# Kernel tuning notes

Measured on AMD Instinct MI355X. Metric: run time of the kernel, lower is better.

## Reference

```python
import jax, jax.numpy as jnp
import numpy as np

FEAT_STRIDE = 16
SCALES = np.array([8.0, 16.0, 32.0])
RATIOS = np.array([0.5, 1.0, 2.0])
PRE_NMS_TOP_N = 6000
POST_NMS_TOP_N = 300
NMS_THRESH = 0.7


def _whctrs(anchor):
    w = anchor[2] - anchor[0] + 1.0
    h = anchor[3] - anchor[1] + 1.0
    cx = anchor[0] + 0.5 * (w - 1.0)
    cy = anchor[1] + 0.5 * (h - 1.0)
    return w, h, cx, cy


def _mkanchors(ws, hs, cx, cy):
    return np.stack([cx - 0.5 * (ws - 1.0), cy - 0.5 * (hs - 1.0),
                     cx + 0.5 * (ws - 1.0), cy + 0.5 * (hs - 1.0)], axis=1)


def generate_anchors(base_size=16, ratios=RATIOS, scales=SCALES):
    base = np.array([0.0, 0.0, base_size - 1.0, base_size - 1.0])
    w, h, cx, cy = _whctrs(base)
    size = w * h
    ws = np.round(np.sqrt(size / ratios))
    hs = np.round(ws * ratios)
    ratio_anchors = _mkanchors(ws, hs, cx, cy)
    out = []
    for a in ratio_anchors:
        w, h, cx, cy = _whctrs(a)
        out.append(_mkanchors(w * scales, h * scales, cx, cy))
    return np.vstack(out)  # (A=9, 4)


def setup_inputs():
    key = jax.random.key(0)
    k1, k2 = jax.random.split(key)
    B, A, H, W = 8, 9, 152, 152
    scores_in = jax.random.normal(k1, (B, 2 * A, H, W), jnp.float32)
    bbox_deltas = 0.5 * jax.random.normal(k2, (B, 4 * A, H, W), jnp.float32)
    im_info = jnp.tile(jnp.array([[H * FEAT_STRIDE, W * FEAT_STRIDE, 1.0]], jnp.float32), (B, 1))
    anchors = jnp.asarray(generate_anchors(), jnp.float32)
    return {"scores_in": scores_in, "bbox_deltas": bbox_deltas, "im_info": im_info, "anchors": anchors}


def bbox_transform_inv(boxes, deltas):
    w = boxes[..., 2] - boxes[..., 0] + 1.0
    h = boxes[..., 3] - boxes[..., 1] + 1.0
    cx = boxes[..., 0] + 0.5 * w
    cy = boxes[..., 1] + 0.5 * h
    dx, dy, dw, dh = deltas[..., 0], deltas[..., 1], deltas[..., 2], deltas[..., 3]
    pcx = dx * w + cx
    pcy = dy * h + cy
    pw = jnp.exp(dw) * w
    ph = jnp.exp(dh) * h
    return jnp.stack([pcx - 0.5 * pw, pcy - 0.5 * ph, pcx + 0.5 * pw, pcy + 0.5 * ph], axis=-1)


def clip_boxes(boxes, im_info):
    wmax = im_info[:, None, 1] - 1.0  # x bound, per image
    hmax = im_info[:, None, 0] - 1.0  # y bound
    x1 = jnp.minimum(jnp.maximum(boxes[..., 0], 0.0), wmax)
    y1 = jnp.minimum(jnp.maximum(boxes[..., 1], 0.0), hmax)
    x2 = jnp.minimum(jnp.maximum(boxes[..., 2], 0.0), wmax)
    y2 = jnp.minimum(jnp.maximum(boxes[..., 3], 0.0), hmax)
    return jnp.stack([x1, y1, x2, y2], axis=-1)


def nms_indices(boxes, thresh, max_out):
    # boxes: (N, 4), sorted by score descending. Greedy NMS -> up to max_out indices, -1 padded.
    x1, y1, x2, y2 = boxes[:, 0], boxes[:, 1], boxes[:, 2], boxes[:, 3]
    areas = (x2 - x1 + 1.0) * (y2 - y1 + 1.0)
    N = boxes.shape[0]

    def body(i, carry):
        suppressed, keep = carry
        idx = jnp.argmax(~suppressed)  # first surviving box = highest remaining score
        valid = ~suppressed[idx]
        keep = keep.at[i].set(jnp.where(valid, idx.astype(jnp.int32), -1))
        xx1 = jnp.maximum(x1[idx], x1)
        yy1 = jnp.maximum(y1[idx], y1)
        xx2 = jnp.minimum(x2[idx], x2)
        yy2 = jnp.minimum(y2[idx], y2)
        inter = jnp.maximum(xx2 - xx1 + 1.0, 0.0) * jnp.maximum(yy2 - yy1 + 1.0, 0.0)
        iou = inter / (areas[idx] + areas - inter)
        suppressed = jnp.where(valid, suppressed | (iou > thresh), suppressed)
        return suppressed, keep

    _, keep = jax.lax.fori_loop(0, max_out, body,
                                (jnp.zeros(N, bool), jnp.full(max_out, -1, jnp.int32)))
    return keep


def _forward(scores_in, bbox_deltas, im_info, anchors):
    B, _, H, W = scores_in.shape
    A = anchors.shape[0]
    # fg objectness scores: channels [A:2A] -> (B, K*A) in (row, col, anchor) order
    scores = scores_in[:, A:].transpose(0, 2, 3, 1).reshape(B, -1)
    deltas = bbox_deltas.transpose(0, 2, 3, 1).reshape(B, -1, 4)
    sx = (jnp.arange(W) * FEAT_STRIDE).astype(jnp.float32)
    sy = (jnp.arange(H) * FEAT_STRIDE).astype(jnp.float32)
    gx, gy = jnp.meshgrid(sx, sy)  # (H, W)
    shifts = jnp.stack([gx.ravel(), gy.ravel(), gx.ravel(), gy.ravel()], axis=1)  # (K, 4)
    all_anchors = (anchors[None, :, :] + shifts[:, None, :]).reshape(-1, 4)  # (K*A, 4)
    proposals = bbox_transform_inv(all_anchors[None], deltas)  # (B, K*A, 4)
    proposals = clip_boxes(proposals, im_info)
    _, order = jax.lax.top_k(scores, PRE_NMS_TOP_N)  # descending, == sorted order truncated
    props_top = jnp.take_along_axis(proposals, order[..., None], axis=1)  # (B, PRE, 4)
    keep = jax.vmap(lambda b: nms_indices(b, NMS_THRESH, POST_NMS_TOP_N))(props_top)  # (B, POST)
    valid = keep >= 0
    sel = jnp.take_along_axis(props_top, jnp.maximum(keep, 0)[..., None], axis=1)
    sel = jnp.where(valid[..., None], sel, 0.0)
    batch_col = jnp.broadcast_to(jnp.arange(B, dtype=jnp.float32)[:, None, None],
                                 (B, POST_NMS_TOP_N, 1))
    return jnp.concatenate([batch_col, sel], axis=2)  # (B, POST, 5)


def reference(scores_in, bbox_deltas, im_info, anchors):
    return _forward(scores_in, bbox_deltas, im_info, anchors)
```

## Files before the change

kernel.cpp:

```cpp
#include <hip/hip_runtime.h>
#include <stdint.h>

#define H_ 152
#define W_ 152
#define A_ 9
#define HW_ (H_ * W_)
#define N_ (HW_ * A_)
#define B_ 8
#define PRE_TOP 6000
#define POST_TOP 300
#define NBUCK 4096
#define NFINE 32768
#define CAND_CAP 8192
#define NMS_TH 0.7f
#define CNT_STRIDE 32
#define RTILE 512
#define DEC_PIXBLK 91
#define DEC_BLKS (72 * DEC_PIXBLK)
#define ZERO_BLKS 128

#define OFF_HIST    0
#define OFF_SSUF    131072
#define OFF_CNT     262144
#define OFF_CAND    263168
#define OFF_GROUP   787456
#define OFF_BOXES   1311744
#define OFF_BALL    2079744
#define WS_NEED     (2079744ull + 26615808ull)


__device__ __forceinline__ unsigned fkey(float f) {
    unsigned u = __float_as_uint(f);
    return (u & 0x80000000u) ? ~u : (u | 0x80000000u);
}

__device__ __forceinline__ bool sup_test(float ax1, float ay1, float ax2, float ay2, float aar,
                                         float bx1, float by1, float bx2, float by2, float bar) {
    float xx1 = fmaxf(ax1, bx1);
    float yy1 = fmaxf(ay1, by1);
    float xx2 = fminf(ax2, bx2);
    float yy2 = fminf(ay2, by2);
    float iw = fmaxf(xx2 - xx1 + 1.0f, 0.0f);
    float ih = fmaxf(yy2 - yy1 + 1.0f, 0.0f);
    float inter = __fmul_rn(iw, ih);
    float iou = inter / (aar + bar - inter);
    return iou > NMS_TH;
}

__device__ __forceinline__ float4 decode_box(float an0, float an1, float an2, float an3,
                                             float sx, float sy,
                                             float dx, float dy, float dw, float dh,
                                             float wmax, float hmax) {
    float ax1 = an0 + sx;
    float ay1 = an1 + sy;
    float ax2 = an2 + sx;
    float ay2 = an3 + sy;
    float ww = ax2 - ax1 + 1.0f;
    float hh = ay2 - ay1 + 1.0f;
    float ctx = ax1 + 0.5f * ww;
    float cty = ay1 + 0.5f * hh;
    float pcx = __fadd_rn(__fmul_rn(dx, ww), ctx);
    float pcy = __fadd_rn(__fmul_rn(dy, hh), cty);
    float pw = __fmul_rn(expf(dw), ww);
    float ph = __fmul_rn(expf(dh), hh);
    float x1 = pcx - 0.5f * pw;
    float y1 = pcy - 0.5f * ph;
    float x2 = pcx + 0.5f * pw;
    float y2 = pcy + 0.5f * ph;
    x1 = fminf(fmaxf(x1, 0.0f), wmax);
    y1 = fminf(fmaxf(y1, 0.0f), hmax);
    x2 = fminf(fmaxf(x2, 0.0f), wmax);
    y2 = fminf(fmaxf(y2, 0.0f), hmax);
    return make_float4(x1, y1, x2, y2);
}


__global__ void init_k(const float* __restrict__ deltas,
                       const float* __restrict__ anchors,
                       const float* __restrict__ im_info,
                       float4* __restrict__ ball,
                       unsigned* __restrict__ zbase, unsigned* __restrict__ zboxes,
                       int nDecBlks) {
    int bid = blockIdx.x;
    if (bid < nDecBlks) {
        int ba = bid / DEC_PIXBLK;
        int b = ba / A_, a = ba - (ba / A_) * A_;
        int pix = (bid % DEC_PIXBLK) * 256 + threadIdx.x;
        if (pix >= HW_) return;
        const float* db = deltas + ((size_t)b * 36 + 4 * a) * HW_;
        float dx = db[pix];
        float dy = db[pix + HW_];
        float dw = db[pix + 2 * HW_];
        float dh = db[pix + 3 * HW_];
        float an0 = anchors[a * 4 + 0];
        float an1 = anchors[a * 4 + 1];
        float an2 = anchors[a * 4 + 2];
        float an3 = anchors[a * 4 + 3];
        float hmax = im_info[b * 3 + 0] - 1.0f;
        float wmax = im_info[b * 3 + 1] - 1.0f;
        int w = pix % W_, h = pix / W_;
        float sx = (float)(w * 16), sy = (float)(h * 16);
        ball[(size_t)b * N_ + a * HW_ + pix] =
            decode_box(an0, an1, an2, an3, sx, sy, dx, dy, dw, dh, wmax, hmax);
    } else {
        const int n1 = 263168 / 4;
        const int n2 = 768000 / 4;
        int i = (bid - nDecBlks) * 256 + (int)threadIdx.x;
        int st = ZERO_BLKS * 256;
        for (int k = i; k < n1 + n2; k += st) {
            if (k < n1) zbase[k] = 0u;
            else zboxes[k - n1] = 0u;
        }
    }
}

__global__ void hist_k(const float* __restrict__ scores, unsigned* __restrict__ hist) {
    __shared__ unsigned lh[NBUCK];
    int b = blockIdx.y;
    for (int i = threadIdx.x; i < NBUCK; i += blockDim.x) lh[i] = 0;
    __syncthreads();
    const float4* sb = (const float4*)(scores + ((size_t)b * 18 + A_) * HW_);
    const int N4 = N_ / 4;
    int stride = gridDim.x * blockDim.x;
    for (int e = blockIdx.x * blockDim.x + threadIdx.x; e < N4; e += stride) {
        float4 v = sb[e];
        atomicAdd(&lh[fkey(v.x) >> 20], 1u);
        atomicAdd(&lh[fkey(v.y) >> 20], 1u);
        atomicAdd(&lh[fkey(v.z) >> 20], 1u);
        atomicAdd(&lh[fkey(v.w) >> 20], 1u);
    }
    __syncthreads();
    for (int i = threadIdx.x; i < NBUCK; i += blockDim.x) {
        unsigned v = lh[i];
        if (v) atomicAdd(&hist[b * NBUCK + i], v);
    }
}

__global__ void scan_k(const unsigned* __restrict__ hist, unsigned* __restrict__ bucketT) {
    __shared__ unsigned ps[1024];
    int b = blockIdx.x, t = threadIdx.x;
    const unsigned* hb = hist + b * NBUCK;
    unsigned c0 = hb[4095 - (4 * t + 0)];
    unsigned c1 = hb[4095 - (4 * t + 1)];
    unsigned c2 = hb[4095 - (4 * t + 2)];
    unsigned c3 = hb[4095 - (4 * t + 3)];
    unsigned local = c0 + c1 + c2 + c3;
    ps[t] = local;
    __syncthreads();
    for (int off = 1; off < 1024; off <<= 1) {
        unsigned v = (t >= off) ? ps[t - off] : 0u;
        __syncthreads();
        ps[t] += v;
        __syncthreads();
    }
    unsigned incl = ps[t], excl = incl - local;
    if (excl < PRE_TOP && incl >= PRE_TOP) {
        unsigned cum = excl;
        unsigned cc[4] = {c0, c1, c2, c3};
#pragma unroll
        for (int k = 0; k < 4; ++k) {
            cum += cc[k];
            if (cum >= PRE_TOP) { bucketT[b] = (unsigned)(4095 - (4 * t + k)); break; }
        }
    }
    if (t == 1023 && ps[1023] < PRE_TOP) bucketT[b] = 0;
}

__global__ void compact_k(const float* __restrict__ scores, const unsigned* __restrict__ bucketT,
                          unsigned* __restrict__ cnt, uint2* __restrict__ cand) {
    __shared__ unsigned wtot[4], wbase[4];
    __shared__ unsigned blkbase;
    int b = blockIdx.y;
    const float4* sb = (const float4*)(scores + ((size_t)b * 18 + A_) * HW_);
    unsigned T = bucketT[b];
    int lane = threadIdx.x & 63;
    int wid = threadIdx.x >> 6;
    const int N4 = N_ / 4;
    int stride = gridDim.x * blockDim.x;
    int niters = (N4 + stride - 1) / stride;
    unsigned long long lower = (lane == 63) ? 0x7fffffffffffffffull
                                            : ((1ull << lane) - 1ull);
    for (int it = 0; it < niters; ++it) {
        int e = it * stride + blockIdx.x * (int)blockDim.x + (int)threadIdx.x;
        bool p0 = false, p1 = false, p2 = false, p3 = false;
        unsigned k0 = 0, k1 = 0, k2 = 0, k3 = 0;
        if (e < N4) {
            float4 v = sb[e];
            k0 = fkey(v.x); k1 = fkey(v.y); k2 = fkey(v.z); k3 = fkey(v.w);
            p0 = (k0 >> 20) >= T; p1 = (k1 >> 20) >= T;
            p2 = (k2 >> 20) >= T; p3 = (k3 >> 20) >= T;
        }
        unsigned long long m0 = __ballot(p0), m1 = __ballot(p1);
        unsigned long long m2 = __ballot(p2), m3 = __ballot(p3);
        unsigned t0 = (unsigned)__popcll(m0), t1 = (unsigned)__popcll(m1);
        unsigned t2 = (unsigned)__popcll(m2), t3 = (unsigned)__popcll(m3);
        unsigned wtotal = t0 + t1 + t2 + t3;
        if (lane == 0) wtot[wid] = wtotal;
        __syncthreads();
        if (threadIdx.x == 0) {
            unsigned s0 = wtot[0], s1 = wtot[1], s2 = wtot[2], s3 = wtot[3];
            unsigned tot = s0 + s1 + s2 + s3;
            blkbase = tot ? atomicAdd(&cnt[b * CNT_STRIDE], tot) : 0u;
            wbase[0] = 0; wbase[1] = s0; wbase[2] = s0 + s1; wbase[3] = s0 + s1 + s2;
        }
        __syncthreads();
        if (wtotal) {
            unsigned base = blkbase + wbase[wid];
            unsigned o0 = base + (unsigned)__popcll(m0 & lower);
            unsigned o1 = base + t0 + (unsigned)__popcll(m1 & lower);
            unsigned o2 = base + t0 + t1 + (unsigned)__popcll(m2 & lower);
            unsigned o3 = base + t0 + t1 + t2 + (unsigned)__popcll(m3 & lower);
            uint2* cb = cand + (size_t)b * CAND_CAP;
            int e4 = e * 4;
            if (p0 && o0 < CAND_CAP) {
                int a = (e4 + 0) / HW_, pix = (e4 + 0) - a * HW_;
                cb[o0] = make_uint2(k0, (unsigned)(pix * A_ + a));
            }
            if (p1 && o1 < CAND_CAP) {
                int a = (e4 + 1) / HW_, pix = (e4 + 1) - a * HW_;
                cb[o1] = make_uint2(k1, (unsigned)(pix * A_ + a));
            }
            if (p2 && o2 < CAND_CAP) {
                int a = (e4 + 2) / HW_, pix = (e4 + 2) - a * HW_;
                cb[o2] = make_uint2(k2, (unsigned)(pix * A_ + a));
            }
            if (p3 && o3 < CAND_CAP) {
                int a = (e4 + 3) / HW_, pix = (e4 + 3) - a * HW_;
                cb[o3] = make_uint2(k3, (unsigned)(pix * A_ + a));
            }
        }
    }
}

__global__ void __launch_bounds__(1024) finesort_k(const unsigned* __restrict__ cnt,
                                                   uint2* __restrict__ cand,
                                                   unsigned long long* __restrict__ grouped) {
    __shared__ unsigned lh[NFINE];
    __shared__ unsigned ps[1024];
    int b = blockIdx.x, t = threadIdx.x;
    int M = min((int)cnt[b * CNT_STRIDE], CAND_CAP);
    uint2* cb = cand + (size_t)b * CAND_CAP;
    unsigned long long* g = grouped + (size_t)b * CAND_CAP;
    for (int i = t; i < NFINE; i += 1024) lh[i] = 0u;
    __syncthreads();
    for (int i = t; i < M; i += 1024) {
        unsigned key16 = cb[i].x >> 16;
        unsigned f = (key16 >= 32768u) ? (key16 - 32768u) : 0u;
        atomicAdd(&lh[f], 1u);
    }
    __syncthreads();
    unsigned c[32];
    unsigned local = 0;
#pragma unroll
    for (int k = 0; k < 32; ++k) { c[k] = lh[32767 - (32 * t + k)]; local += c[k]; }
    ps[t] = local;
    __syncthreads();
    for (int off = 1; off < 1024; off <<= 1) {
        unsigned v = (t >= off) ? ps[t - off] : 0u;
        __syncthreads();
        ps[t] += v;
        __syncthreads();
    }
    unsigned run = ps[t] - local;
    __syncthreads();
#pragma unroll
    for (int k = 0; k < 32; ++k) {
        lh[32767 - (32 * t + k)] = run;
        run += c[k];
    }
    __syncthreads();
    for (int i = t; i < M; i += 1024) {
        uint2 cd = cb[i];
        unsigned key16 = cd.x >> 16;
        unsigned f = (key16 >= 32768u) ? (key16 - 32768u) : 0u;
        unsigned pos = atomicAdd(&lh[f], 1u);
        if (pos < CAND_CAP)
            g[pos] = ((unsigned long long)cd.x << 32) | (unsigned)(~cd.y);
    }
    __syncthreads();
    ushort* S16 = (ushort*)cb;
    for (int i = t; i < NFINE; i += 1024)
        S16[i] = (ushort)min(lh[i], 65535u);
}

__global__ void __launch_bounds__(256) rank_k(const unsigned* __restrict__ cnt,
                                              const unsigned long long* __restrict__ grouped,
                                              const ushort* __restrict__ S16all,
                                              const float4* __restrict__ ball,
                                              float4* __restrict__ boxes) {
    __shared__ unsigned long long tile[RTILE];
    __shared__ int s_rs, s_re;
    int b = blockIdx.y, t = threadIdx.x;
    int M = min((int)cnt[b * CNT_STRIDE], CAND_CAP);
    int c0 = blockIdx.x * 256;
    if (c0 >= M) return;
    const unsigned long long* g = grouped + (size_t)b * CAND_CAP;
    const ushort* S16 = S16all + (size_t)b * NFINE;
    int i = c0 + t;
    bool valid = i < M;
    unsigned long long comp = valid ? g[i] : 0ull;

    unsigned n = valid ? ~(unsigned)comp : 0u;
    int a = (int)(n % A_);
    int pix = (int)(n / A_);
    float4 pre = make_float4(0.f, 0.f, 0.f, 0.f);
    if (valid) pre = ball[(size_t)b * N_ + a * HW_ + pix];

    unsigned key16 = (unsigned)(comp >> 48);
    int f = (key16 >= 32768u) ? (int)(key16 - 32768u) : 0;
    int bs = 0, be = 0;
    if (valid) {
        bs = (f < 32767) ? min((int)S16[f + 1], M) : 0;
        be = min((int)S16[f], M);
    }
    if (t == 0) {
        unsigned kf = (unsigned)(g[c0] >> 48);
        int bf = (kf >= 32768u) ? (int)(kf - 32768u) : 0;
        int last = min(c0 + 255, M - 1);
        unsigned kl = (unsigned)(g[last] >> 48);
        int bl = (kl >= 32768u) ? (int)(kl - 32768u) : 0;
        s_rs = (bf < 32767) ? min((int)S16[bf + 1], M) : 0;
        s_re = min((int)S16[bl], M);
    }
    __syncthreads();
    int rs = s_rs, re = s_re;
    int cgt = 0;
    for (int tb = rs; tb < re; tb += RTILE) {
        int navail = min(RTILE, re - tb);
        __syncthreads();
        for (int j = t; j < navail; j += 256) tile[j] = g[tb + j];
        __syncthreads();
        if (valid) {
            int lo = max(bs, tb) - tb;
            int hi = min(be, tb + navail) - tb;
            int a0 = 0, a1 = 0, a2 = 0, a3 = 0, a4 = 0, a5 = 0, a6 = 0, a7 = 0;
            int j = lo;
            for (; j + 8 <= hi; j += 8) {
                unsigned long long v0 = tile[j + 0];
                unsigned long long v1 = tile[j + 1];
                unsigned long long v2 = tile[j + 2];
                unsigned long long v3 = tile[j + 3];
                unsigned long long v4 = tile[j + 4];
                unsigned long long v5 = tile[j + 5];
                unsigned long long v6 = tile[j + 6];
                unsigned long long v7 = tile[j + 7];
                a0 += (v0 > comp); a1 += (v1 > comp); a2 += (v2 > comp); a3 += (v3 > comp);
                a4 += (v4 > comp); a5 += (v5 > comp); a6 += (v6 > comp); a7 += (v7 > comp);
            }
            for (; j < hi; ++j) cgt += (tile[j] > comp);
            cgt += (a0 + a1 + a2 + a3) + (a4 + a5 + a6 + a7);
        }
    }
    if (!valid) return;
    int rank = bs + cgt;
    if (rank >= PRE_TOP) return;
    boxes[(size_t)b * PRE_TOP + rank] = pre;
}

__global__ void __launch_bounds__(1024) nms_k(const float4* __restrict__ boxes,
                                              float* __restrict__ out) {
    __shared__ float4 kbox[POST_TOP];
    __shared__ float  karea[POST_TOP];
    __shared__ float4 gbox4[64];
    __shared__ float  gar[64];
    __shared__ unsigned extw[2];
    __shared__ unsigned intraw[128];
    __shared__ unsigned long long s_keep;
    __shared__ int s_base, s_kc, s_done;
    int b = blockIdx.x, t = threadIdx.x;
    int lane = t & 63, w = t >> 6;
    if (t == 0) { s_kc = 0; s_done = 0; }
    const float4* bb = boxes + (size_t)b * PRE_TOP;
    const int ngroups = (PRE_TOP + 63) / 64;

    float4 vcur = make_float4(0.f, 0.f, 0.f, 0.f);
    if (t < 64) vcur = bb[t];

    for (int g = 0; g < ngroups; ++g) {
        __syncthreads();
        if (s_done) break;
        int gbase = g * 64;
        int gsz = min(64, PRE_TOP - gbase);
        if (t < gsz) {
            gbox4[t] = vcur;
            gar[t] = __fmul_rn(vcur.z - vcur.x + 1.0f, vcur.w - vcur.y + 1.0f);
        }
        if (t < 64) {
            int nidx = min(gbase + 64 + t, PRE_TOP - 1);
            vcur = bb[nidx];
        }
        if (t < 2) extw[t] = 0u;
        if (t < 128) intraw[t] = 0u;
        __syncthreads();

        int kc = s_kc;
        {
            int j = t >> 4, sub = t & 15;
            if (j < gsz) {
                float4 cb4 = gbox4[j];
                float car = gar[j];
                bool any = false;
                for (int kk = sub; kk < kc && !any; kk += 16) {
                    float4 kb = kbox[kk];
                    float ka = karea[kk];
                    any = sup_test(kb.x, kb.y, kb.z, kb.w, ka,
                                   cb4.x, cb4.y, cb4.z, cb4.w, car);
                }
                if (any) atomicOr(&extw[j >> 5], 1u << (j & 31));
            }
        }
        {
            float4 mb = gbox4[lane];
            float mar = gar[lane];
#pragma unroll
            for (int it = 0; it < 4; ++it) {
                int jj = w + it * 16;
                float4 bj = gbox4[jj];
                float baj = gar[jj];
                bool sup = (jj < lane) && (lane < gsz) && (jj < gsz) &&
                           sup_test(bj.x, bj.y, bj.z, bj.w, baj,
                                    mb.x, mb.y, mb.z, mb.w, mar);
                unsigned long long m = __ballot(sup);
                if (lane == 0 && (unsigned)m) atomicOr(&intraw[2 * jj], (unsigned)m);
                if (lane == 1 && (unsigned)(m >> 32))
                    atomicOr(&intraw[2 * jj + 1], (unsigned)(m >> 32));
            }
        }
        __syncthreads();

        if (t == 0) {
            unsigned long long ext64 = (unsigned long long)extw[0] |
                                       ((unsigned long long)extw[1] << 32);
            unsigned long long validm = (gsz >= 64) ? ~0ull : ((1ull << gsz) - 1ull);
            unsigned long long alive = (~ext64) & validm;
            unsigned long long keep = 0ull;
            int kcc = s_kc;
            s_base = kcc;
            while (alive && kcc < POST_TOP) {
                int j = __ffsll((long long)alive) - 1;
                keep |= (1ull << j);
                ++kcc;
                unsigned long long row = (unsigned long long)intraw[2 * j] |
                                         ((unsigned long long)intraw[2 * j + 1] << 32);
                alive &= ~row;
                alive &= ~(1ull << j);
            }
            s_keep = keep;
            s_kc = kcc;
            if (kcc >= POST_TOP) s_done = 1;
        }
        __syncthreads();

        if (t < gsz && ((s_keep >> t) & 1ull)) {
            int rank = __popcll(s_keep & ((1ull << t) - 1ull));
            int slot = s_base + rank;
            float4 mb = gbox4[t];
            kbox[slot] = mb;
            karea[slot] = gar[t];
            float* o = out + (size_t)(b * POST_TOP + slot) * 5;
            o[0] = (float)b; o[1] = mb.x; o[2] = mb.y; o[3] = mb.z; o[4] = mb.w;
        }
    }
    __syncthreads();
    for (int sl = s_kc + t; sl < POST_TOP; sl += 1024) {
        float* o = out + (size_t)(b * POST_TOP + sl) * 5;
        o[0] = (float)b; o[1] = 0.f; o[2] = 0.f; o[3] = 0.f; o[4] = 0.f;
    }
}


extern "C" void kernel_launch(void* const* d_in, const int* in_sizes, int n_in,
                              void* d_out, int out_size, void* d_ws, size_t ws_size,
                              hipStream_t stream) {
    const float* scores  = (const float*)d_in[0];
    const float* deltas  = (const float*)d_in[1];
    const float* im_info = (const float*)d_in[2];
    const float* anchors = (const float*)d_in[3];
    float* out = (float*)d_out;

    unsigned*           hist    = (unsigned*)((char*)d_ws + OFF_HIST);
    unsigned*           cnt     = (unsigned*)((char*)d_ws + OFF_CNT);
    uint2*              cand    = (uint2*)((char*)d_ws + OFF_CAND);
    unsigned long long* grouped = (unsigned long long*)((char*)d_ws + OFF_GROUP);
    float4*             boxes   = (float4*)((char*)d_ws + OFF_BOXES);
    float4*             ball    = (float4*)((char*)d_ws + OFF_BALL);
    unsigned*           bucketT = cnt + B_ * CNT_STRIDE - 8;

    init_k<<<DEC_BLKS + ZERO_BLKS, 256, 0, stream>>>(deltas, anchors, im_info, ball,
                                                     (unsigned*)d_ws,
                                                     (unsigned*)((char*)d_ws + OFF_BOXES),
                                                     DEC_BLKS);
    hist_k<<<dim3(64, B_), 256, 0, stream>>>(scores, hist);
    scan_k<<<B_, 1024, 0, stream>>>(hist, bucketT);
    compact_k<<<dim3(64, B_), 256, 0, stream>>>(scores, bucketT, cnt, cand);
    finesort_k<<<B_, 1024, 0, stream>>>(cnt, cand, grouped);
    rank_k<<<dim3(32, B_), 256, 0, stream>>>(cnt, grouped, (const ushort*)cand, ball, boxes);
    nms_k<<<B_, 1024, 0, stream>>>(boxes, out);
}
```

Measured before the change: 93.90 us.

## Fuse score histogram into decode kernel and zero workspace with memset

Folds the per-image score histogram blocks into the box-decode launch as extra blocks, so histogramming and decoding run concurrently and one kernel launch goes away. The in-kernel zeroing of the histogram and counter region becomes a hipMemsetAsync. The explicit zeroing of the boxes workspace region is dropped, which is only safe if later stages overwrite every slot. Every block of the fused kernel now reserves 16 KB of shared memory, decode blocks included, which may reduce occupancy for the decode path.

Result: slower. 97.48 us (+3.8%).

```diff
diff --git a/kernel.cpp b/kernel.cpp
--- a/kernel.cpp
+++ b/kernel.cpp
@@ -17,7 +17,8 @@
 #define RTILE 512
 #define DEC_PIXBLK 91
 #define DEC_BLKS (72 * DEC_PIXBLK)
-#define ZERO_BLKS 128
+#define HIST_BLKS_PER_B 64
+#define HIST_BLKS (HIST_BLKS_PER_B * B_)
 
 #define OFF_HIST    0
 #define OFF_SSUF    131072
@@ -75,14 +76,15 @@
 }
 
 
-__global__ void init_k(const float* __restrict__ deltas,
-                       const float* __restrict__ anchors,
-                       const float* __restrict__ im_info,
-                       float4* __restrict__ ball,
-                       unsigned* __restrict__ zbase, unsigned* __restrict__ zboxes,
-                       int nDecBlks) {
+__global__ void init_hist_k(const float* __restrict__ deltas,
+                            const float* __restrict__ anchors,
+                            const float* __restrict__ im_info,
+                            const float* __restrict__ scores,
+                            float4* __restrict__ ball,
+                            unsigned* __restrict__ hist) {
+    __shared__ unsigned lh[NBUCK];
     int bid = blockIdx.x;
-    if (bid < nDecBlks) {
+    if (bid < DEC_BLKS) {
         int ba = bid / DEC_PIXBLK;
         int b = ba / A_, a = ba - (ba / A_) * A_;
         int pix = (bid % DEC_PIXBLK) * 256 + threadIdx.x;
@@ -103,36 +105,28 @@
         ball[(size_t)b * N_ + a * HW_ + pix] =
             decode_box(an0, an1, an2, an3, sx, sy, dx, dy, dw, dh, wmax, hmax);
     } else {
-        const int n1 = 263168 / 4;
-        const int n2 = 768000 / 4;
-        int i = (bid - nDecBlks) * 256 + (int)threadIdx.x;
-        int st = ZERO_BLKS * 256;
-        for (int k = i; k < n1 + n2; k += st) {
-            if (k < n1) zbase[k] = 0u;
-            else zboxes[k - n1] = 0u;
-        }
-    }
-}
-
-__global__ void hist_k(const float* __restrict__ scores, unsigned* __restrict__ hist) {
-    __shared__ unsigned lh[NBUCK];
-    int b = blockIdx.y;
-    for (int i = threadIdx.x; i < NBUCK; i += blockDim.x) lh[i] = 0;
-    __syncthreads();
-    const float4* sb = (const float4*)(scores + ((size_t)b * 18 + A_) * HW_);
-    const int N4 = N_ / 4;
-    int stride = gridDim.x * blockDim.x;
-    for (int e = blockIdx.x * blockDim.x + threadIdx.x; e < N4; e += stride) {
-        float4 v = sb[e];
-        atomicAdd(&lh[fkey(v.x) >> 20], 1u);
-        atomicAdd(&lh[fkey(v.y) >> 20], 1u);
-        atomicAdd(&lh[fkey(v.z) >> 20], 1u);
-        atomicAdd(&lh[fkey(v.w) >> 20], 1u);
-    }
-    __syncthreads();
-    for (int i = threadIdx.x; i < NBUCK; i += blockDim.x) {
-        unsigned v = lh[i];
-        if (v) atomicAdd(&hist[b * NBUCK + i], v);
+        int bid2 = bid - DEC_BLKS;
+        int b = bid2 >> 6;
+        int bx = bid2 & 63;
+        int t = threadIdx.x;
+        for (int i = t; i < NBUCK; i += 256) lh[i] = 0;
+        __syncthreads();
+        const float4* sb = (const float4*)(scores + ((size_t)b * 18 + A_) * HW_);
+        const int N4 = N_ / 4;
+        const int stride = HIST_BLKS_PER_B * 256;
+        for (int e = bx * 256 + t; e < N4; e += stride) {
+            float4 v = sb[e];
+            atomicAdd(&lh[fkey(v.x) >> 20], 1u);
+            atomicAdd(&lh[fkey(v.y) >> 20], 1u);
+            atomicAdd(&lh[fkey(v.z) >> 20], 1u);
+            atomicAdd(&lh[fkey(v.w) >> 20], 1u);
+        }
+        __syncthreads();
+        unsigned* hb = hist + b * NBUCK;
+        for (int i = t; i < NBUCK; i += 256) {
+            unsigned v = lh[i];
+            if (v) atomicAdd(&hb[i], v);
+        }
     }
 }
 
@@ -486,11 +480,9 @@
     float4*             ball    = (float4*)((char*)d_ws + OFF_BALL);
     unsigned*           bucketT = cnt + B_ * CNT_STRIDE - 8;
 
-    init_k<<<DEC_BLKS + ZERO_BLKS, 256, 0, stream>>>(deltas, anchors, im_info, ball,
-                                                     (unsigned*)d_ws,
-                                                     (unsigned*)((char*)d_ws + OFF_BOXES),
-                                                     DEC_BLKS);
-    hist_k<<<dim3(64, B_), 256, 0, stream>>>(scores, hist);
+    hipMemsetAsync(d_ws, 0, 263168, stream);
+    init_hist_k<<<DEC_BLKS + HIST_BLKS, 256, 0, stream>>>(deltas, anchors, im_info,
+                                                          scores, ball, hist);
     scan_k<<<B_, 1024, 0, stream>>>(hist, bucketT);
     compact_k<<<dim3(64, B_), 256, 0, stream>>>(scores, bucketT, cnt, cand);
     finesort_k<<<B_, 1024, 0, stream>>>(cnt, cand, grouped);
```
